# Optimization experiments

Hardware: AMD Instinct MI355X
Metric: run time of the kernel (lower is better)

The kernel has to match this reference:

```python
import jax, jax.numpy as jnp
import numpy as np

H = 8          # num_heads
D = 64         # head_dim
IN = 512       # input_dim
SCALE = D ** -0.5


def setup_inputs() -> dict:
    key = jax.random.key(0)
    ks = jax.random.split(key, 5)
    b, n = 4, 2048
    inner = H * D
    x = jax.random.normal(ks[0], (b, n, IN), dtype=jnp.float32)
    # nn.Linear weights stored as [out, in]; apply as x @ W.T
    Wq = jax.random.normal(ks[1], (inner, IN), dtype=jnp.float32) * (IN ** -0.5)
    Wkv = jax.random.normal(ks[2], (2 * inner, IN), dtype=jnp.float32) * (IN ** -0.5)
    Wo = jax.random.normal(ks[3], (IN, inner), dtype=jnp.float32) * (inner ** -0.5)
    bo = jax.random.normal(ks[4], (IN,), dtype=jnp.float32) * 0.01
    return {"x": x, "Wq": Wq, "Wkv": Wkv, "Wo": Wo, "bo": bo}


def reference(x, Wq, Wkv, Wo, bo):
    b, n, _ = x.shape
    q = jnp.einsum('bni,oi->bno', x, Wq).reshape(b, n, H, D).transpose(0, 2, 1, 3)
    kv = jnp.einsum('bni,oi->bno', x, Wkv)
    k, v = jnp.split(kv, 2, axis=-1)
    k = k.reshape(b, n, H, D).transpose(0, 2, 1, 3)
    v = v.reshape(b, n, H, D).transpose(0, 2, 1, 3)
    attn = jax.nn.softmax(jnp.einsum('bhnd,bhmd->bhnm', q, k) * SCALE, axis=-1)
    # dropout in eval mode: identity
    out = jnp.einsum('bhnm,bhmd->bhnd', attn, v)
    out = out.transpose(0, 2, 1, 3).reshape(b, n, H * D)
    return jnp.einsum('bno,io->bni', out, Wo) + bo
```

## Files before the change

### kernel.cpp

```cpp
#include <hip/hip_runtime.h>
#include <hip/hip_bf16.h>

#define H_ 8
#define D_ 64
#define IN_ 512
#define B_ 4
#define N_ 2048
#define TOK_ (B_*N_)
#define CLOG2_ 0.18033688011112042f

typedef __attribute__((ext_vector_type(8))) short short8;
typedef __attribute__((ext_vector_type(4))) short bs4;
typedef __attribute__((ext_vector_type(4))) float f32x4;

__device__ __forceinline__ unsigned short f2bf(float f) {
  unsigned int u = __float_as_uint(f);
  u += 0x7FFFu + ((u >> 16) & 1u);
  return (unsigned short)(u >> 16);
}

__device__ __forceinline__ short8 cvt8(const float4 a, const float4 b) {
  union { short8 v; __hip_bfloat162 h[4]; } z;
  z.h[0] = __float22bfloat162_rn(make_float2(a.x, a.y));
  z.h[1] = __float22bfloat162_rn(make_float2(a.z, a.w));
  z.h[2] = __float22bfloat162_rn(make_float2(b.x, b.y));
  z.h[3] = __float22bfloat162_rn(make_float2(b.z, b.w));
  return z.v;
}

__device__ __forceinline__ bs4 pack4(float a, float b, float c, float d) {
  union { bs4 v; __hip_bfloat162 h[2]; } z;
  z.h[0] = __float22bfloat162_rn(make_float2(a, b));
  z.h[1] = __float22bfloat162_rn(make_float2(c, d));
  return z.v;
}

__device__ __forceinline__ void gld16(const unsigned short* g, unsigned short* l) {
  __builtin_amdgcn_global_load_lds(
      (const __attribute__((address_space(1))) void*)g,
      (__attribute__((address_space(3))) void*)l, 16, 0, 0);
}

__global__ __launch_bounds__(256) void conv_kernel(
    const float* __restrict__ src, unsigned short* __restrict__ dst)
{
  size_t i = ((size_t)blockIdx.x * 256 + threadIdx.x) * 8;
  float4 a = *(const float4*)(src + i);
  float4 b = *(const float4*)(src + i + 4);
  *(short8*)(dst + i) = cvt8(a, b);
}

__global__ __launch_bounds__(256) void qkv_gemm_kernel(
    const unsigned short* __restrict__ xbf, const unsigned short* __restrict__ wbf,
    unsigned short* __restrict__ qws, unsigned short* __restrict__ kws,
    unsigned short* __restrict__ vws)
{
  __shared__ __attribute__((aligned(16))) unsigned short sm[128 * 136];
  unsigned short* sA = sm;
  unsigned short* sB = sm + 8192;

  const int t0 = blockIdx.x * 128;
  const int c0 = blockIdx.y * 128;
  const int cls = c0 >> 9;

  const int tid = threadIdx.x;
  const int wave = tid >> 6, lane = tid & 63;
  const int quad = lane >> 4, l16 = lane & 15;
  const int wm = wave >> 1, wn = wave & 1;

  const int r_ = tid >> 3;
  const int gc = (tid & 7) ^ (r_ & 7);
  const unsigned short* abase = xbf + (size_t)(t0 + r_) * IN_ + gc * 8;
  const unsigned short* bbase = wbf + (size_t)(c0 + r_) * IN_ + gc * 8;

  f32x4 acc[4][4];
  #pragma unroll
  for (int i = 0; i < 4; i++)
    #pragma unroll
    for (int j = 0; j < 4; j++) acc[i][j] = (f32x4){0.f, 0.f, 0.f, 0.f};

  for (int k0 = 0; k0 < IN_; k0 += 64) {
    #pragma unroll
    for (int i = 0; i < 4; i++) {
      gld16(abase + (size_t)i * 32 * IN_ + k0, sA + (i * 256 + tid) * 8);
      gld16(bbase + (size_t)i * 32 * IN_ + k0, sB + (i * 256 + tid) * 8);
    }
    __syncthreads();

    #pragma unroll
    for (int kc = 0; kc < 2; kc++) {
      const int sw = (((kc * 4 + quad) ^ (l16 & 7)) << 3);
      short8 af[4], bf[4];
      #pragma unroll
      for (int mi = 0; mi < 4; mi++)
        af[mi] = *(const short8*)&sA[(wm * 64 + mi * 16 + l16) * 64 + sw];
      #pragma unroll
      for (int ni = 0; ni < 4; ni++)
        bf[ni] = *(const short8*)&sB[(wn * 64 + ni * 16 + l16) * 64 + sw];
      #pragma unroll
      for (int mi = 0; mi < 4; mi++)
        #pragma unroll
        for (int ni = 0; ni < 4; ni++)
          acc[mi][ni] = __builtin_amdgcn_mfma_f32_16x16x32_bf16(af[mi], bf[ni], acc[mi][ni], 0, 0, 0);
    }
    __syncthreads();
  }

  if (cls < 2) {
    const float qs = (cls == 0) ? CLOG2_ : 1.0f;
    #pragma unroll
    for (int mi = 0; mi < 4; mi++) {
      const int row0 = wm * 64 + mi * 16 + quad * 4;
      #pragma unroll
      for (int ni = 0; ni < 4; ni++) {
        const int col = wn * 64 + ni * 16 + l16;
        #pragma unroll
        for (int r = 0; r < 4; r++)
          sm[(row0 + r) * 136 + col] = f2bf(acc[mi][ni][r] * qs);
      }
    }
    __syncthreads();
    const int row = tid >> 1, half = tid & 1;
    const int t = t0 + row, bb = t >> 11, nn = t & (N_ - 1);
    const int cw = (c0 & 511) + half * 64;
    const int hh = cw >> 6;
    unsigned short* dst = ((cls == 0) ? qws : kws) +
                          ((size_t)(bb * H_ + hh) * N_ + nn) * D_;
    const unsigned short* srcp = &sm[row * 136 + half * 64];
    #pragma unroll
    for (int j = 0; j < 8; j++)
      *(uint4*)(dst + j * 8) = *(const uint4*)(srcp + j * 8);
  } else {
    #pragma unroll
    for (int mi = 0; mi < 4; mi++) {
      const int tk = wm * 64 + mi * 16 + quad * 4;
      #pragma unroll
      for (int ni = 0; ni < 4; ni++) {
        const int col = wn * 64 + ni * 16 + l16;
        bs4 pk4 = pack4(acc[mi][ni][0], acc[mi][ni][1], acc[mi][ni][2], acc[mi][ni][3]);
        *(bs4*)&sm[col * 136 + tk] = pk4;
      }
    }
    __syncthreads();
    const int col = tid >> 1, half = tid & 1;
    const int cw = (c0 - 1024) + col;
    const int hh = cw >> 6, dd = cw & 63;
    const int bb = t0 >> 11, n0 = (t0 & (N_ - 1)) + half * 64;
    unsigned short* dst = vws + ((size_t)(bb * H_ + hh) * D_ + dd) * N_ + n0;
    const unsigned short* srcp = &sm[col * 136 + half * 64];
    #pragma unroll
    for (int j = 0; j < 8; j++)
      *(uint4*)(dst + j * 8) = *(const uint4*)(srcp + j * 8);
  }
}

__global__ __launch_bounds__(256) void attention_kernel(
    const unsigned short* __restrict__ qws,
    const unsigned short* __restrict__ kws,
    const unsigned short* __restrict__ vws,
    unsigned short* __restrict__ ows)
{
  __shared__ __attribute__((aligned(16))) unsigned short sm[2][8192];

  const int q0 = blockIdx.x * 64;
  const int bh = blockIdx.y;
  const int tid = threadIdx.x;
  const int wave = tid >> 6, lane = tid & 63;
  const int quad = lane >> 4, l16 = lane & 15;

  const unsigned short* qbase = qws + (size_t)bh * N_ * D_;
  const unsigned short* kbase = kws + (size_t)bh * N_ * D_;
  const unsigned short* vbase = vws + (size_t)bh * D_ * N_;

  const int qrow = q0 + wave * 16 + l16;
  short8 qf[2];
  #pragma unroll
  for (int kc = 0; kc < 2; kc++)
    qf[kc] = *(const short8*)(qbase + (size_t)qrow * D_ + kc * 32 + quad * 8);

  f32x4 ot[4];
  f32x4 otl;
  #pragma unroll
  for (int db = 0; db < 4; db++) ot[db] = (f32x4){0.f, 0.f, 0.f, 0.f};
  otl = (f32x4){0.f, 0.f, 0.f, 0.f};
  const bs4 ones4 = {(short)0x3F80, (short)0x3F80, (short)0x3F80, (short)0x3F80};

  const int r_ = tid >> 3;
  const int gc = (tid & 7) ^ (r_ & 7);
  const unsigned short* kst = kbase + (size_t)r_ * D_ + gc * 8;
  const unsigned short* vst = vbase + (size_t)r_ * N_ + gc * 8;

  {
    unsigned short* Ks = &sm[0][0];
    unsigned short* Vs = &sm[0][4096];
    gld16(kst,                 Ks + tid * 8);
    gld16(kst + 32 * D_,       Ks + 2048 + tid * 8);
    gld16(vst,                 Vs + tid * 8);
    gld16(vst + 32 * N_,       Vs + 2048 + tid * 8);
  }

  for (int kt = 0; kt < N_ / 64; kt++) {
    const int cur = kt & 1;
    __syncthreads();
    if (kt + 1 < N_ / 64) {
      const int k0 = (kt + 1) * 64;
      unsigned short* Ks = &sm[cur ^ 1][0];
      unsigned short* Vs = &sm[cur ^ 1][4096];
      gld16(kst + (size_t)k0 * D_,            Ks + tid * 8);
      gld16(kst + (size_t)(k0 + 32) * D_,     Ks + 2048 + tid * 8);
      gld16(vst + k0,                         Vs + tid * 8);
      gld16(vst + k0 + 32 * N_,               Vs + 2048 + tid * 8);
    }
    const unsigned short* Ks = &sm[cur][0];
    const unsigned short* Vs = &sm[cur][4096];

    f32x4 st[4];
    #pragma unroll
    for (int nb = 0; nb < 4; nb++) st[nb] = (f32x4){0.f, 0.f, 0.f, 0.f};
    #pragma unroll
    for (int kc = 0; kc < 2; kc++) {
      const int sw = (((kc * 4 + quad) ^ (l16 & 7)) << 3);
      #pragma unroll
      for (int nb = 0; nb < 4; nb++) {
        short8 kf = *(const short8*)&Ks[(nb * 16 + l16) * 64 + sw];
        st[nb] = __builtin_amdgcn_mfma_f32_16x16x32_bf16(kf, qf[kc], st[nb], 0, 0, 0);
      }
    }

    bs4 pf[4];
    #pragma unroll
    for (int nb = 0; nb < 4; nb++) {
      float p0 = __builtin_amdgcn_exp2f(st[nb][0]);
      float p1 = __builtin_amdgcn_exp2f(st[nb][1]);
      float p2 = __builtin_amdgcn_exp2f(st[nb][2]);
      float p3 = __builtin_amdgcn_exp2f(st[nb][3]);
      pf[nb] = pack4(p0, p1, p2, p3);
    }

    #pragma unroll
    for (int kb = 0; kb < 4; kb++) {
      const int g = kb * 2 + (quad >> 1);
      const int sub = (quad & 1) * 4;
      bs4 vf[4];
      #pragma unroll
      for (int db = 0; db < 4; db++)
        vf[db] = *(const bs4*)&Vs[(db * 16 + l16) * 64 + ((g ^ (l16 & 7)) << 3) + sub];
      #pragma unroll
      for (int db = 0; db < 4; db++)
        ot[db] = __builtin_amdgcn_mfma_f32_16x16x16bf16_1k(vf[db], pf[kb], ot[db], 0, 0, 0);
      otl = __builtin_amdgcn_mfma_f32_16x16x16bf16_1k(ones4, pf[kb], otl, 0, 0, 0);
    }
  }

  const float inv = 1.f / otl[0];
  __syncthreads();
  unsigned short* Os = (unsigned short*)sm;
  #pragma unroll
  for (int db = 0; db < 4; db++) {
    bs4 pk4 = pack4(ot[db][0] * inv, ot[db][1] * inv, ot[db][2] * inv, ot[db][3] * inv);
    *(bs4*)&Os[(wave * 16 + l16) * 72 + db * 16 + quad * 4] = pk4;
  }
  __syncthreads();
  const int b_ = bh >> 3, h_ = bh & 7;
  const int qloc = tid >> 2, chunk = tid & 3;
  unsigned short* dst = ows + ((size_t)b_ * N_ + q0 + qloc) * (H_ * D_) + h_ * 64 + chunk * 16;
  const unsigned short* srcp = &Os[qloc * 72 + chunk * 16];
  *(uint4*)dst = *(const uint4*)srcp;
  *(uint4*)(dst + 8) = *(const uint4*)(srcp + 8);
}

__global__ __launch_bounds__(256) void out_gemm_kernel(
    const unsigned short* __restrict__ ain, const unsigned short* __restrict__ wobf,
    const float* __restrict__ bo, float* __restrict__ y)
{
  __shared__ __attribute__((aligned(16))) unsigned short sm[12288];
  unsigned short* sA = sm;
  unsigned short* sB = sm + 8192;

  const int t0 = blockIdx.x * 128;
  const int c0 = blockIdx.y * 64;
  const int tid = threadIdx.x;
  const int wave = tid >> 6, lane = tid & 63;
  const int quad = lane >> 4, l16 = lane & 15;

  const int r_ = tid >> 3;
  const int gc = (tid & 7) ^ (r_ & 7);
  const unsigned short* abase = ain  + (size_t)(t0 + r_) * IN_ + gc * 8;
  const unsigned short* bbase = wobf + (size_t)(c0 + r_) * IN_ + gc * 8;

  f32x4 acc[2][4];
  #pragma unroll
  for (int i = 0; i < 2; i++)
    #pragma unroll
    for (int j = 0; j < 4; j++) acc[i][j] = (f32x4){0.f, 0.f, 0.f, 0.f};

  for (int k0 = 0; k0 < IN_; k0 += 64) {
    #pragma unroll
    for (int i = 0; i < 4; i++)
      gld16(abase + (size_t)i * 32 * IN_ + k0, sA + (i * 256 + tid) * 8);
    #pragma unroll
    for (int i = 0; i < 2; i++)
      gld16(bbase + (size_t)i * 32 * IN_ + k0, sB + (i * 256 + tid) * 8);
    __syncthreads();

    #pragma unroll
    for (int kc = 0; kc < 2; kc++) {
      const int sw = (((kc * 4 + quad) ^ (l16 & 7)) << 3);
      short8 af[2], bf[4];
      #pragma unroll
      for (int mi = 0; mi < 2; mi++)
        af[mi] = *(const short8*)&sA[(wave * 32 + mi * 16 + l16) * 64 + sw];
      #pragma unroll
      for (int ni = 0; ni < 4; ni++)
        bf[ni] = *(const short8*)&sB[(ni * 16 + l16) * 64 + sw];
      #pragma unroll
      for (int mi = 0; mi < 2; mi++)
        #pragma unroll
        for (int ni = 0; ni < 4; ni++)
          acc[mi][ni] = __builtin_amdgcn_mfma_f32_16x16x32_bf16(af[mi], bf[ni], acc[mi][ni], 0, 0, 0);
    }
    __syncthreads();
  }

  #pragma unroll
  for (int mi = 0; mi < 2; mi++) {
    const int t = t0 + wave * 32 + mi * 16 + quad * 4;
    #pragma unroll
    for (int ni = 0; ni < 4; ni++) {
      const int c = c0 + ni * 16 + l16;
      const float bias = bo[c];
      float* dst = y + (size_t)t * IN_ + c;
      dst[0]        = acc[mi][ni][0] + bias;
      dst[IN_]      = acc[mi][ni][1] + bias;
      dst[2 * IN_]  = acc[mi][ni][2] + bias;
      dst[3 * IN_]  = acc[mi][ni][3] + bias;
    }
  }
}

extern "C" void kernel_launch(void* const* d_in, const int* in_sizes, int n_in,
                              void* d_out, int out_size, void* d_ws, size_t ws_size,
                              hipStream_t stream) {
  const float* x   = (const float*)d_in[0];
  const float* Wq  = (const float*)d_in[1];
  const float* Wkv = (const float*)d_in[2];
  const float* Wo  = (const float*)d_in[3];
  const float* bo  = (const float*)d_in[4];
  float* out = (float*)d_out;

  unsigned short* qws  = (unsigned short*)d_ws;
  unsigned short* kws  = qws + (size_t)TOK_ * 512;
  unsigned short* vws  = kws + (size_t)TOK_ * 512;
  unsigned short* ows  = vws + (size_t)TOK_ * 512;
  unsigned short* wbf  = ows + (size_t)TOK_ * 512;
  unsigned short* wobf = wbf + (size_t)1536 * 512;
  unsigned short* xbf  = ows;

  conv_kernel<<<dim3(TOK_ * IN_ / 2048), 256, 0, stream>>>(x, xbf);
  conv_kernel<<<dim3(512 * 512 / 2048), 256, 0, stream>>>(Wq, wbf);
  conv_kernel<<<dim3(1024 * 512 / 2048), 256, 0, stream>>>(Wkv, wbf + 512 * 512);
  conv_kernel<<<dim3(512 * 512 / 2048), 256, 0, stream>>>(Wo, wobf);
  qkv_gemm_kernel<<<dim3(TOK_ / 128, 1536 / 128), 256, 0, stream>>>(xbf, wbf, qws, kws, vws);
  attention_kernel<<<dim3(N_ / 64, B_ * H_), 256, 0, stream>>>(qws, kws, vws, ows);
  out_gemm_kernel<<<dim3(TOK_ / 128, 512 / 64), 256, 0, stream>>>(ows, wobf, bo, out);
}
```

Baseline: 175.6 us.

## Double-buffer GEMM K tiles and merge four conversion kernels into one launch

Both projection GEMMs now step through K in tiles of 32 instead of 64, using two LDS buffers. Each iteration issues the async global-to-LDS load for the next tile before computing on the current one, and the loop needs only one barrier instead of two. The LDS swizzle is changed to match the 32-wide rows. The four fp32-to-bf16 conversion launches are merged into a single kernel that picks its source by block index, which removes launch overhead. The cost is more loop iterations with fewer MFMAs each, and the single barrier has to be correct for the buffer reuse.

```diff
diff --git a/kernel.cpp b/kernel.cpp
--- a/kernel.cpp
+++ b/kernel.cpp
@@ -41,13 +41,24 @@
       (__attribute__((address_space(3))) void*)l, 16, 0, 0);
 }
 
-__global__ __launch_bounds__(256) void conv_kernel(
-    const float* __restrict__ src, unsigned short* __restrict__ dst)
+__global__ __launch_bounds__(256) void conv_all_kernel(
+    const float* __restrict__ x, const float* __restrict__ Wq,
+    const float* __restrict__ Wkv, const float* __restrict__ Wo,
+    unsigned short* __restrict__ xbf, unsigned short* __restrict__ wbf,
+    unsigned short* __restrict__ wobf)
 {
-  size_t i = ((size_t)blockIdx.x * 256 + threadIdx.x) * 8;
+  const int b = blockIdx.x;
+  const float* src;
+  unsigned short* dst;
+  size_t base;
+  if (b < 2048)      { src = x;   dst = xbf;             base = (size_t)b * 2048; }
+  else if (b < 2176) { src = Wq;  dst = wbf;             base = (size_t)(b - 2048) * 2048; }
+  else if (b < 2432) { src = Wkv; dst = wbf + 512 * 512; base = (size_t)(b - 2176) * 2048; }
+  else               { src = Wo;  dst = wobf;            base = (size_t)(b - 2432) * 2048; }
+  size_t i = base + (size_t)threadIdx.x * 8;
   float4 a = *(const float4*)(src + i);
-  float4 b = *(const float4*)(src + i + 4);
-  *(short8*)(dst + i) = cvt8(a, b);
+  float4 c = *(const float4*)(src + i + 4);
+  *(short8*)(dst + i) = cvt8(a, c);
 }
 
 __global__ __launch_bounds__(256) void qkv_gemm_kernel(
@@ -56,8 +67,6 @@
     unsigned short* __restrict__ vws)
 {
   __shared__ __attribute__((aligned(16))) unsigned short sm[128 * 136];
-  unsigned short* sA = sm;
-  unsigned short* sB = sm + 8192;
 
   const int t0 = blockIdx.x * 128;
   const int c0 = blockIdx.y * 128;
@@ -68,43 +77,50 @@
   const int quad = lane >> 4, l16 = lane & 15;
   const int wm = wave >> 1, wn = wave & 1;
 
-  const int r_ = tid >> 3;
-  const int gc = (tid & 7) ^ (r_ & 7);
+  const int r_ = tid >> 2;
+  const int gc = (tid & 3) ^ (r_ & 3);
   const unsigned short* abase = xbf + (size_t)(t0 + r_) * IN_ + gc * 8;
   const unsigned short* bbase = wbf + (size_t)(c0 + r_) * IN_ + gc * 8;
 
+  auto stage = [&](int k0, int buf) {
+    unsigned short* sA = sm + buf * 8192;
+    unsigned short* sB = sA + 4096;
+    gld16(abase + k0,            sA + tid * 8);
+    gld16(abase + 64 * IN_ + k0, sA + 2048 + tid * 8);
+    gld16(bbase + k0,            sB + tid * 8);
+    gld16(bbase + 64 * IN_ + k0, sB + 2048 + tid * 8);
+  };
+
   f32x4 acc[4][4];
   #pragma unroll
   for (int i = 0; i < 4; i++)
     #pragma unroll
     for (int j = 0; j < 4; j++) acc[i][j] = (f32x4){0.f, 0.f, 0.f, 0.f};
 
-  for (int k0 = 0; k0 < IN_; k0 += 64) {
-    #pragma unroll
-    for (int i = 0; i < 4; i++) {
-      gld16(abase + (size_t)i * 32 * IN_ + k0, sA + (i * 256 + tid) * 8);
-      gld16(bbase + (size_t)i * 32 * IN_ + k0, sB + (i * 256 + tid) * 8);
-    }
-    __syncthreads();
-
-    #pragma unroll
-    for (int kc = 0; kc < 2; kc++) {
-      const int sw = (((kc * 4 + quad) ^ (l16 & 7)) << 3);
-      short8 af[4], bf[4];
-      #pragma unroll
-      for (int mi = 0; mi < 4; mi++)
-        af[mi] = *(const short8*)&sA[(wm * 64 + mi * 16 + l16) * 64 + sw];
+  stage(0, 0);
+
+  for (int kt = 0; kt < 16; kt++) {
+    const int cur = kt & 1;
+    __syncthreads();
+    if (kt + 1 < 16) stage((kt + 1) * 32, cur ^ 1);
+    const unsigned short* sA = sm + cur * 8192;
+    const unsigned short* sB = sA + 4096;
+    const int sw = ((quad ^ (l16 & 3)) << 3);
+    short8 af[4], bf[4];
+    #pragma unroll
+    for (int mi = 0; mi < 4; mi++)
+      af[mi] = *(const short8*)&sA[(wm * 64 + mi * 16 + l16) * 32 + sw];
+    #pragma unroll
+    for (int ni = 0; ni < 4; ni++)
+      bf[ni] = *(const short8*)&sB[(wn * 64 + ni * 16 + l16) * 32 + sw];
+    #pragma unroll
+    for (int mi = 0; mi < 4; mi++)
       #pragma unroll
       for (int ni = 0; ni < 4; ni++)
-        bf[ni] = *(const short8*)&sB[(wn * 64 + ni * 16 + l16) * 64 + sw];
-      #pragma unroll
-      for (int mi = 0; mi < 4; mi++)
-        #pragma unroll
-        for (int ni = 0; ni < 4; ni++)
-          acc[mi][ni] = __builtin_amdgcn_mfma_f32_16x16x32_bf16(af[mi], bf[ni], acc[mi][ni], 0, 0, 0);
-    }
-    __syncthreads();
-  }
+        acc[mi][ni] = __builtin_amdgcn_mfma_f32_16x16x32_bf16(af[mi], bf[ni], acc[mi][ni], 0, 0, 0);
+  }
+
+  __syncthreads();
 
   if (cls < 2) {
     const float qs = (cls == 0) ? CLOG2_ : 1.0f;
@@ -274,8 +290,6 @@
     const float* __restrict__ bo, float* __restrict__ y)
 {
   __shared__ __attribute__((aligned(16))) unsigned short sm[12288];
-  unsigned short* sA = sm;
-  unsigned short* sB = sm + 8192;
 
   const int t0 = blockIdx.x * 128;
   const int c0 = blockIdx.y * 64;
@@ -283,43 +297,46 @@
   const int wave = tid >> 6, lane = tid & 63;
   const int quad = lane >> 4, l16 = lane & 15;
 
-  const int r_ = tid >> 3;
-  const int gc = (tid & 7) ^ (r_ & 7);
+  const int r_ = tid >> 2;
+  const int gc = (tid & 3) ^ (r_ & 3);
   const unsigned short* abase = ain  + (size_t)(t0 + r_) * IN_ + gc * 8;
   const unsigned short* bbase = wobf + (size_t)(c0 + r_) * IN_ + gc * 8;
 
+  auto stage = [&](int k0, int buf) {
+    unsigned short* sA = sm + buf * 6144;
+    unsigned short* sB = sA + 4096;
+    gld16(abase + k0,            sA + tid * 8);
+    gld16(abase + 64 * IN_ + k0, sA + 2048 + tid * 8);
+    gld16(bbase + k0,            sB + tid * 8);
+  };
+
   f32x4 acc[2][4];
   #pragma unroll
   for (int i = 0; i < 2; i++)
     #pragma unroll
     for (int j = 0; j < 4; j++) acc[i][j] = (f32x4){0.f, 0.f, 0.f, 0.f};
 
-  for (int k0 = 0; k0 < IN_; k0 += 64) {
-    #pragma unroll
-    for (int i = 0; i < 4; i++)
-      gld16(abase + (size_t)i * 32 * IN_ + k0, sA + (i * 256 + tid) * 8);
-    #pragma unroll
-    for (int i = 0; i < 2; i++)
-      gld16(bbase + (size_t)i * 32 * IN_ + k0, sB + (i * 256 + tid) * 8);
-    __syncthreads();
-
-    #pragma unroll
-    for (int kc = 0; kc < 2; kc++) {
-      const int sw = (((kc * 4 + quad) ^ (l16 & 7)) << 3);
-      short8 af[2], bf[4];
-      #pragma unroll
-      for (int mi = 0; mi < 2; mi++)
-        af[mi] = *(const short8*)&sA[(wave * 32 + mi * 16 + l16) * 64 + sw];
+  stage(0, 0);
+
+  for (int kt = 0; kt < 16; kt++) {
+    const int cur = kt & 1;
+    __syncthreads();
+    if (kt + 1 < 16) stage((kt + 1) * 32, cur ^ 1);
+    const unsigned short* sA = sm + cur * 6144;
+    const unsigned short* sB = sA + 4096;
+    const int sw = ((quad ^ (l16 & 3)) << 3);
+    short8 af[2], bf[4];
+    #pragma unroll
+    for (int mi = 0; mi < 2; mi++)
+      af[mi] = *(const short8*)&sA[(wave * 32 + mi * 16 + l16) * 32 + sw];
+    #pragma unroll
+    for (int ni = 0; ni < 4; ni++)
+      bf[ni] = *(const short8*)&sB[(ni * 16 + l16) * 32 + sw];
+    #pragma unroll
+    for (int mi = 0; mi < 2; mi++)
       #pragma unroll
       for (int ni = 0; ni < 4; ni++)
-        bf[ni] = *(const short8*)&sB[(ni * 16 + l16) * 64 + sw];
-      #pragma unroll
-      for (int mi = 0; mi < 2; mi++)
-        #pragma unroll
-        for (int ni = 0; ni < 4; ni++)
-          acc[mi][ni] = __builtin_amdgcn_mfma_f32_16x16x32_bf16(af[mi], bf[ni], acc[mi][ni], 0, 0, 0);
-    }
-    __syncthreads();
+        acc[mi][ni] = __builtin_amdgcn_mfma_f32_16x16x32_bf16(af[mi], bf[ni], acc[mi][ni], 0, 0, 0);
   }
 
   #pragma unroll
@@ -356,10 +373,7 @@
   unsigned short* wobf = wbf + (size_t)1536 * 512;
   unsigned short* xbf  = ows;
 
-  conv_kernel<<<dim3(TOK_ * IN_ / 2048), 256, 0, stream>>>(x, xbf);
-  conv_kernel<<<dim3(512 * 512 / 2048), 256, 0, stream>>>(Wq, wbf);
-  conv_kernel<<<dim3(1024 * 512 / 2048), 256, 0, stream>>>(Wkv, wbf + 512 * 512);
-  conv_kernel<<<dim3(512 * 512 / 2048), 256, 0, stream>>>(Wo, wobf);
+  conv_all_kernel<<<dim3(2560), 256, 0, stream>>>(x, Wq, Wkv, Wo, xbf, wbf, wobf);
   qkv_gemm_kernel<<<dim3(TOK_ / 128, 1536 / 128), 256, 0, stream>>>(xbf, wbf, qws, kws, vws);
   attention_kernel<<<dim3(N_ / 64, B_ * H_), 256, 0, stream>>>(qws, kws, vws, ows);
   out_gemm_kernel<<<dim3(TOK_ / 128, 512 / 64), 256, 0, stream>>>(ows, wobf, bo, out);
```

Measured after the change: 169.3 us. 1.04x faster.
